# Kernel tuning notes

Hardware: AMD Instinct MI355X
Metric: run time of the kernel (lower is better)

## Reference

```python
import jax, jax.numpy as jnp
import numpy as np

N = 100000
E = 1600000
IN_FEATS = 256
OUT_FEATS = 256
EPS_WSUM = 1e-8   # clamp for weight sum
EPS_NORM = 1e-12  # F.normalize eps


def setup_inputs() -> dict:
    key = jax.random.key(0)
    k1, k2, k3, k4, k5 = jax.random.split(key, 5)
    x = jax.random.normal(k1, (N, IN_FEATS), dtype=jnp.float32)
    edge_index = jax.random.randint(k2, (2, E), 0, N, dtype=jnp.int64)
    edge_weight = jax.random.uniform(k3, (E,), dtype=jnp.float32)
    # Xavier-uniform-like init scale for [out, in] weights
    lim = float(np.sqrt(6.0 / (IN_FEATS + OUT_FEATS)) * np.sqrt(2.0))
    W_self = jax.random.uniform(k4, (OUT_FEATS, IN_FEATS), dtype=jnp.float32, minval=-lim, maxval=lim)
    W_neigh = jax.random.uniform(k5, (OUT_FEATS, IN_FEATS), dtype=jnp.float32, minval=-lim, maxval=lim)
    bias = jnp.zeros((OUT_FEATS,), dtype=jnp.float32)
    return {"x": x, "edge_index": edge_index, "edge_weight": edge_weight,
            "W_self": W_self, "W_neigh": W_neigh, "bias": bias}


def reference(x, edge_index, edge_weight, W_self, W_neigh, bias):
    row, col = edge_index[0], edge_index[1]
    # weighted mean aggregation: gather -> scale -> scatter-add -> normalize by weight sum
    weighted = x[row] * edge_weight[:, None]                       # [E, in]
    num = jax.ops.segment_sum(weighted, col, num_segments=N)       # [N, in]
    wsum = jax.ops.segment_sum(edge_weight, col, num_segments=N)   # [N]
    wsum = jnp.maximum(wsum, EPS_WSUM)
    neigh = num / wsum[:, None]                                    # [N, in]
    out = x @ W_self.T + neigh @ W_neigh.T + bias                  # [N, out]
    # L2 normalize (torch F.normalize semantics)
    nrm = jnp.maximum(jnp.linalg.norm(out, axis=-1, keepdims=True), EPS_NORM)
    return out / nrm
```

## Files before the change

### kernel.cpp

```cpp
#include <hip/hip_runtime.h>
#include <hip/hip_bf16.h>
#include <stdint.h>

#define IN_F 256
#define K_TOT 512
#define GR 64

typedef __attribute__((ext_vector_type(8))) _Float16 f16x8;
typedef __attribute__((ext_vector_type(4))) _Float16 f16x4;
typedef __attribute__((ext_vector_type(4))) float f32x4;
typedef __attribute__((ext_vector_type(2))) float f32x2;

#if __has_builtin(__builtin_amdgcn_cvt_pk_f32_fp8) && __has_builtin(__builtin_amdgcn_cvt_pk_fp8_f32)
#define HW_FP8 1
#endif

__device__ __forceinline__ float fp8_dec1(uint32_t b) {
  union { uint16_t u; _Float16 h; } cv;
  cv.u = (uint16_t)((b & 0x7F) << 7);
  float v = (float)cv.h * 256.0f;
  return (b & 0x80) ? -v : v;
}
__device__ __forceinline__ uint32_t fp8_enc1(float f) {
  union { _Float16 h; uint16_t u; } cv;
  cv.h = (_Float16)(f * (1.0f / 256.0f));
  uint32_t s = (cv.u >> 8) & 0x80;
  uint32_t t = cv.u & 0x7FFF;
  uint32_t r = (t + 0x3F + ((t >> 7) & 1)) >> 7;
  if (r > 0x7E) r = 0x7E;
  return s | r;
}
__device__ __forceinline__ void fp8x4_dec(uint32_t w, float4& o) {
#ifdef HW_FP8
  f32x2 lo = __builtin_amdgcn_cvt_pk_f32_fp8((int)w, false);
  f32x2 hi = __builtin_amdgcn_cvt_pk_f32_fp8((int)w, true);
  o.x = lo[0]; o.y = lo[1]; o.z = hi[0]; o.w = hi[1];
#else
  o.x = fp8_dec1(w & 0xFF); o.y = fp8_dec1((w >> 8) & 0xFF);
  o.z = fp8_dec1((w >> 16) & 0xFF); o.w = fp8_dec1(w >> 24);
#endif
}
__device__ __forceinline__ uint32_t fp8x4_enc(float a, float b, float c, float d) {
#ifdef HW_FP8
  int r = __builtin_amdgcn_cvt_pk_fp8_f32(a, b, 0, false);
  r = __builtin_amdgcn_cvt_pk_fp8_f32(c, d, r, true);
  return (uint32_t)r;
#else
  return fp8_enc1(a) | (fp8_enc1(b) << 8) | (fp8_enc1(c) << 16) | (fp8_enc1(d) << 24);
#endif
}

__global__ void init_kernel(const float* __restrict__ x,
                            const float* __restrict__ Ws,
                            const float* __restrict__ Wn,
                            const int* __restrict__ ei,
                            _Float16* __restrict__ Bhi,
                            uint32_t* __restrict__ xq, _Float16* __restrict__ Af16,
                            int* __restrict__ counts,
                            int* __restrict__ flag, int N, int nconv, int nmem) {
  __shared__ int bad_s[256];
  const int b = blockIdx.x;
  const int t = threadIdx.x;
  if (b < 512) {
    int idx = b * 256 + t;
    int j = idx >> 9;
    int k = idx & 511;
    float v = (k < IN_F) ? Ws[j * IN_F + k] : Wn[j * IN_F + (k - IN_F)];
    size_t addr = ((size_t)(k >> 5) * 256 + j) * 32 + (k & 31);
    Bhi[addr] = (_Float16)v;
  } else if (b < 512 + nconv) {
    size_t base = (size_t)(b - 512) * 4096 + (size_t)t * 16;
    size_t tot = (size_t)N * IN_F;
    if (base + 16 <= tot) {
      const float4* x4 = reinterpret_cast<const float4*>(x + base);
      float4 v0 = x4[0], v1 = x4[1], v2 = x4[2], v3 = x4[3];
      uint4 o;
      o.x = fp8x4_enc(v0.x, v0.y, v0.z, v0.w);
      o.y = fp8x4_enc(v1.x, v1.y, v1.z, v1.w);
      o.z = fp8x4_enc(v2.x, v2.y, v2.z, v2.w);
      o.w = fp8x4_enc(v3.x, v3.y, v3.z, v3.w);
      *reinterpret_cast<uint4*>(xq + base / 4) = o;
      size_t row = base >> 8;
      int col = (int)(base & 255);
      f16x8 h0 = {(_Float16)v0.x, (_Float16)v0.y, (_Float16)v0.z, (_Float16)v0.w,
                  (_Float16)v1.x, (_Float16)v1.y, (_Float16)v1.z, (_Float16)v1.w};
      f16x8 h1 = {(_Float16)v2.x, (_Float16)v2.y, (_Float16)v2.z, (_Float16)v2.w,
                  (_Float16)v3.x, (_Float16)v3.y, (_Float16)v3.z, (_Float16)v3.w};
      _Float16* dst = Af16 + row * K_TOT + col;
      *reinterpret_cast<f16x8*>(dst) = h0;
      *reinterpret_cast<f16x8*>(dst + 8) = h1;
    }
  } else if (b < 512 + nconv + nmem) {
    int base = (b - 512 - nconv) * 1024 + t * 4;
#pragma unroll
    for (int j = 0; j < 4; ++j)
      if (base + j < N) counts[base + j] = 0;
  } else {
    int bad = 0;
#pragma unroll
    for (int p = 0; p < 8; ++p) {
      int i = t + p * 256;
      if (ei[2 * i + 1] != 0) bad = 1;
    }
    bad_s[t] = bad;
    __syncthreads();
    for (int s = 128; s > 0; s >>= 1) {
      if (t < s) bad_s[t] |= bad_s[t + s];
      __syncthreads();
    }
    if (t == 0) *flag = (bad_s[0] == 0) ? 1 : 0;
  }
}

__global__ void hist_kernel(const int* __restrict__ ei, const int* __restrict__ flag,
                            int* __restrict__ counts, int E) {
  int e = blockIdx.x * 256 + threadIdx.x;
  if (e >= E) return;
  int is64 = *flag;
  int dst = is64 ? ei[2 * (E + e)] : ei[E + e];
  atomicAdd(counts + dst, 1);
}

__global__ void scan1_kernel(const int* __restrict__ counts, int* __restrict__ offsets,
                             int* __restrict__ bsums, int N) {
  __shared__ int buf[1024];
  int t = threadIdx.x;
  int i = blockIdx.x * 1024 + t;
  int v = (i < N) ? counts[i] : 0;
  buf[t] = v;
  __syncthreads();
  for (int s = 1; s < 1024; s <<= 1) {
    int add = (t >= s) ? buf[t - s] : 0;
    __syncthreads();
    buf[t] += add;
    __syncthreads();
  }
  if (i < N) offsets[i] = buf[t] - v;
  if (t == 1023) bsums[blockIdx.x] = buf[1023];
}

__global__ void scan23_kernel(int* __restrict__ offsets, const int* __restrict__ bsums,
                              int* __restrict__ cursor, int N, int E, int nb) {
  __shared__ int sb[128];
  int t = threadIdx.x;
  int v = 0;
  if (t < 128) {
    v = (t < nb) ? bsums[t] : 0;
    sb[t] = v;
  }
  __syncthreads();
  for (int s = 1; s < 128; s <<= 1) {
    int add = 0;
    if (t < 128 && t >= s) add = sb[t - s];
    __syncthreads();
    if (t < 128) sb[t] += add;
    __syncthreads();
  }
  if (t < 128) sb[t] -= v;
  __syncthreads();
  int i = blockIdx.x * 256 + t;
  if (i < N) {
    int o = offsets[i] + sb[i >> 10];
    offsets[i] = o;
    cursor[i] = o;
  }
  if (i == 0) offsets[N] = E;
}

__global__ void fill_kernel(const int* __restrict__ ei, const float* __restrict__ ew,
                            const int* __restrict__ flag, int* __restrict__ cursor,
                            uint32_t* __restrict__ edges, int E, int nper) {
  int q = blockIdx.x & 7;
  int e = (blockIdx.x >> 3) * 256 + threadIdx.x;
  if (e >= E) return;
  int is64 = *flag;
  int dst = is64 ? ei[2 * (E + e)] : ei[E + e];
  if (dst / nper != q) return;
  int src = is64 ? ei[2 * e] : ei[e];
  uint32_t w15 = (uint32_t)__float2int_rn(ew[e] * 32767.0f);
  int pos = atomicAdd(cursor + dst, 1);
  edges[pos] = ((uint32_t)src << 15) | w15;
}

__launch_bounds__(256)
__global__ void aggregate_fp8_kernel(const uint32_t* __restrict__ xq,
                                     const int* __restrict__ offsets,
                                     const uint32_t* __restrict__ edges,
                                     _Float16* __restrict__ Af16, int N) {
  int wid = blockIdx.x * 4 + (threadIdx.x >> 6);
  if (wid >= N) return;
  int lane = threadIdx.x & 63;
  int beg = offsets[wid];
  int end = offsets[wid + 1];
  float4 acc = {0.f, 0.f, 0.f, 0.f};
  float ws = 0.f;
  const float wscale = 1.0f / 32767.0f;
  int e = beg;
  for (; e + 3 < end; e += 4) {
    uint32_t n0 = edges[e], n1 = edges[e + 1], n2 = edges[e + 2], n3 = edges[e + 3];
    float w0 = (float)(n0 & 0x7FFF) * wscale, w1 = (float)(n1 & 0x7FFF) * wscale;
    float w2 = (float)(n2 & 0x7FFF) * wscale, w3 = (float)(n3 & 0x7FFF) * wscale;
    uint32_t q0 = xq[(size_t)(n0 >> 15) * 64 + lane];
    uint32_t q1 = xq[(size_t)(n1 >> 15) * 64 + lane];
    uint32_t q2 = xq[(size_t)(n2 >> 15) * 64 + lane];
    uint32_t q3 = xq[(size_t)(n3 >> 15) * 64 + lane];
    float4 f0, f1, f2, f3;
    fp8x4_dec(q0, f0); fp8x4_dec(q1, f1); fp8x4_dec(q2, f2); fp8x4_dec(q3, f3);
    acc.x += f0.x * w0 + f1.x * w1 + f2.x * w2 + f3.x * w3;
    acc.y += f0.y * w0 + f1.y * w1 + f2.y * w2 + f3.y * w3;
    acc.z += f0.z * w0 + f1.z * w1 + f2.z * w2 + f3.z * w3;
    acc.w += f0.w * w0 + f1.w * w1 + f2.w * w2 + f3.w * w3;
    ws += w0 + w1 + w2 + w3;
  }
  for (; e < end; ++e) {
    uint32_t n0 = edges[e];
    float w0 = (float)(n0 & 0x7FFF) * wscale;
    uint32_t q0 = xq[(size_t)(n0 >> 15) * 64 + lane];
    float4 f0;
    fp8x4_dec(q0, f0);
    acc.x += f0.x * w0; acc.y += f0.y * w0; acc.z += f0.z * w0; acc.w += f0.w * w0;
    ws += w0;
  }
  float inv = 1.f / fmaxf(ws, 1e-8f);
  f16x4 o = {(_Float16)(acc.x * inv), (_Float16)(acc.y * inv),
             (_Float16)(acc.z * inv), (_Float16)(acc.w * inv)};
  *reinterpret_cast<f16x4*>(Af16 + (size_t)wid * K_TOT + IN_F + lane * 4) = o;
}

__launch_bounds__(256)
__global__ void gemm_norm_kernel(const _Float16* __restrict__ Af16,
                                 const _Float16* __restrict__ Bhi,
                                 const float* __restrict__ bias,
                                 float* __restrict__ out, int N) {
  const int t = threadIdx.x;
  const int lane = t & 63;
  const int w = t >> 6;
  const int row0 = blockIdx.x * GR;

  __shared__ _Float16 Ah[2][256 * 8];
  __shared__ float ssb[GR][4];

  f32x4 acc[4][4];
#pragma unroll
  for (int rt = 0; rt < 4; ++rt)
#pragma unroll
    for (int ct = 0; ct < 4; ++ct) acc[rt][ct] = (f32x4){0.f, 0.f, 0.f, 0.f};

  int st_row = row0 + (t >> 6) * 16 + (t & 15);
  if (st_row >= N) st_row = N - 1;
  const _Float16* Abase = Af16 + (size_t)st_row * K_TOT + ((t >> 4) & 3) * 8;

  const size_t bfrag = (size_t)(w * 64 + (lane & 15)) * 32 + (lane >> 4) * 8;
  const _Float16* BhiP = Bhi + bfrag;

  *reinterpret_cast<f16x8*>(&Ah[0][t * 8]) = *reinterpret_cast<const f16x8*>(Abase);
  f16x8 a_next = *reinterpret_cast<const f16x8*>(Abase + 32);
  f16x8 bH[2][4];
#pragma unroll
  for (int ct = 0; ct < 4; ++ct) {
    bH[0][ct] = *reinterpret_cast<const f16x8*>(BhiP + ct * 512);
    bH[1][ct] = *reinterpret_cast<const f16x8*>(BhiP + 8192 + ct * 512);
  }
  __syncthreads();

#pragma unroll
  for (int ks = 0; ks < 16; ++ks) {
    f16x8 aH[4];
#pragma unroll
    for (int rt = 0; rt < 4; ++rt)
      aH[rt] = *reinterpret_cast<const f16x8*>(&Ah[ks & 1][(rt * 64 + lane) * 8]);
    f16x8 bNext[4];
    if (ks < 14) {
#pragma unroll
      for (int ct = 0; ct < 4; ++ct)
        bNext[ct] = *reinterpret_cast<const f16x8*>(BhiP + (size_t)(ks + 2) * 8192 + ct * 512);
    }
    if (ks < 15)
      *reinterpret_cast<f16x8*>(&Ah[(ks + 1) & 1][t * 8]) = a_next;
    if (ks < 14)
      a_next = *reinterpret_cast<const f16x8*>(Abase + (size_t)(ks + 2) * 32);
#pragma unroll
    for (int ct = 0; ct < 4; ++ct)
#pragma unroll
      for (int rt = 0; rt < 4; ++rt)
        acc[rt][ct] = __builtin_amdgcn_mfma_f32_16x16x32_f16(aH[rt], bH[ks & 1][ct], acc[rt][ct], 0, 0, 0);
    if (ks < 14) {
#pragma unroll
      for (int ct = 0; ct < 4; ++ct) bH[ks & 1][ct] = bNext[ct];
    }
    __syncthreads();
  }

  float bv[4];
#pragma unroll
  for (int ct = 0; ct < 4; ++ct) bv[ct] = bias[w * 64 + ct * 16 + (lane & 15)];

#pragma unroll
  for (int rt = 0; rt < 4; ++rt)
#pragma unroll
    for (int i = 0; i < 4; ++i) {
      float ssv = 0.f;
#pragma unroll
      for (int ct = 0; ct < 4; ++ct) {
        float val = acc[rt][ct][i] + bv[ct];
        acc[rt][ct][i] = val;
        ssv += val * val;
      }
#pragma unroll
      for (int s = 1; s < 16; s <<= 1) ssv += __shfl_xor(ssv, s, 64);
      if ((lane & 15) == 0) ssb[rt * 16 + (lane >> 4) * 4 + i][w] = ssv;
    }
  __syncthreads();

#pragma unroll
  for (int rt = 0; rt < 4; ++rt)
#pragma unroll
    for (int i = 0; i < 4; ++i) {
      int rl = rt * 16 + (lane >> 4) * 4 + i;
      f32x4 s4 = *reinterpret_cast<const f32x4*>(&ssb[rl][0]);
      float ss = s4[0] + s4[1] + s4[2] + s4[3];
      int gr = row0 + rl;
      if (gr < N) {
        float scale = 1.0f / fmaxf(sqrtf(ss), 1e-12f);
#pragma unroll
        for (int ct = 0; ct < 4; ++ct)
          out[(size_t)gr * IN_F + w * 64 + ct * 16 + (lane & 15)] = acc[rt][ct][i] * scale;
      }
    }
}

extern "C" void kernel_launch(void* const* d_in, const int* in_sizes, int n_in,
                              void* d_out, int out_size, void* d_ws, size_t ws_size,
                              hipStream_t stream) {
  const float* x = (const float*)d_in[0];
  const int* ei = (const int*)d_in[1];
  const float* ew = (const float*)d_in[2];
  const float* Wself = (const float*)d_in[3];
  const float* Wneigh = (const float*)d_in[4];
  const float* bias = (const float*)d_in[5];
  float* out = (float*)d_out;

  const int N = in_sizes[0] / IN_F;
  const int E = in_sizes[2];

  char* p = (char*)d_ws;
  _Float16* Af16 = (_Float16*)p;     p += (size_t)N * K_TOT * 2;
  _Float16* Bhi = (_Float16*)p;      p += (size_t)K_TOT * IN_F * 2;
  uint32_t* xq = (uint32_t*)p;       p += (size_t)N * IN_F;
  uint32_t* edges = (uint32_t*)p;    p += (size_t)E * 4;
  int* counts = (int*)p;             p += (size_t)N * 4;
  int* offsets = (int*)p;            p += (size_t)(N + 1) * 4;
  int* cursor = (int*)p;             p += (size_t)N * 4;
  int* bsums = (int*)p;              p += 128 * 4;
  int* flag = (int*)p;

  const int nconv = (int)(((size_t)N * IN_F + 4095) / 4096);
  const int nmem = (N + 1023) / 1024;
  const int nb = (N + 1023) / 1024;
  const int nper = (N + 7) / 8;

  init_kernel<<<512 + nconv + nmem + 1, 256, 0, stream>>>(
      x, Wself, Wneigh, ei, Bhi, xq, Af16, counts, flag, N, nconv, nmem);
  hist_kernel<<<(E + 255) / 256, 256, 0, stream>>>(ei, flag, counts, E);
  scan1_kernel<<<nb, 1024, 0, stream>>>(counts, offsets, bsums, N);
  scan23_kernel<<<(N + 255) / 256, 256, 0, stream>>>(offsets, bsums, cursor, N, E, nb);
  fill_kernel<<<((E + 255) / 256) * 8, 256, 0, stream>>>(ei, ew, flag, cursor, edges,
                                                         E, nper);
  aggregate_fp8_kernel<<<(N + 3) / 4, 256, 0, stream>>>(xq, offsets, edges, Af16, N);
  gemm_norm_kernel<<<(N + GR - 1) / GR, 256, 0, stream>>>(Af16, Bhi, bias, out, N);
}
```

Measured before the change: 302.8 us.

## Fuse neighbor aggregation into GEMM kernel, keeping aggregated rows in LDS

Merges the aggregation and GEMM+normalize kernels into one. Each block first aggregates neighbor features for its 64 rows into a shared-memory tile, then runs the MFMA GEMM reading the self half from fp32 x (converted to fp16 on the fly) and the neighbor half from LDS. This removes the fp16 Af16 intermediate buffer: its write in init, its write in aggregation, and its re-read in GEMM. The cost is that the gather phase runs with fewer resident waves per CU (GEMM-sized blocks with extra LDS), which can reduce latency hiding for the random xq loads. The gather loop is also unrolled to 8 edges per iteration.

```diff
diff --git a/kernel.cpp b/kernel.cpp
--- a/kernel.cpp
+++ b/kernel.cpp
@@ -55,7 +55,7 @@
                             const float* __restrict__ Wn,
                             const int* __restrict__ ei,
                             _Float16* __restrict__ Bhi,
-                            uint32_t* __restrict__ xq, _Float16* __restrict__ Af16,
+                            uint32_t* __restrict__ xq,
                             int* __restrict__ counts,
                             int* __restrict__ flag, int N, int nconv, int nmem) {
   __shared__ int bad_s[256];
@@ -80,15 +80,6 @@
       o.z = fp8x4_enc(v2.x, v2.y, v2.z, v2.w);
       o.w = fp8x4_enc(v3.x, v3.y, v3.z, v3.w);
       *reinterpret_cast<uint4*>(xq + base / 4) = o;
-      size_t row = base >> 8;
-      int col = (int)(base & 255);
-      f16x8 h0 = {(_Float16)v0.x, (_Float16)v0.y, (_Float16)v0.z, (_Float16)v0.w,
-                  (_Float16)v1.x, (_Float16)v1.y, (_Float16)v1.z, (_Float16)v1.w};
-      f16x8 h1 = {(_Float16)v2.x, (_Float16)v2.y, (_Float16)v2.z, (_Float16)v2.w,
-                  (_Float16)v3.x, (_Float16)v3.y, (_Float16)v3.z, (_Float16)v3.w};
-      _Float16* dst = Af16 + row * K_TOT + col;
-      *reinterpret_cast<f16x8*>(dst) = h0;
-      *reinterpret_cast<f16x8*>(dst + 8) = h1;
     }
   } else if (b < 512 + nconv + nmem) {
     int base = (b - 512 - nconv) * 1024 + t * 4;
@@ -183,62 +174,65 @@
 }
 
 __launch_bounds__(256)
-__global__ void aggregate_fp8_kernel(const uint32_t* __restrict__ xq,
-                                     const int* __restrict__ offsets,
-                                     const uint32_t* __restrict__ edges,
-                                     _Float16* __restrict__ Af16, int N) {
-  int wid = blockIdx.x * 4 + (threadIdx.x >> 6);
-  if (wid >= N) return;
-  int lane = threadIdx.x & 63;
-  int beg = offsets[wid];
-  int end = offsets[wid + 1];
-  float4 acc = {0.f, 0.f, 0.f, 0.f};
-  float ws = 0.f;
-  const float wscale = 1.0f / 32767.0f;
-  int e = beg;
-  for (; e + 3 < end; e += 4) {
-    uint32_t n0 = edges[e], n1 = edges[e + 1], n2 = edges[e + 2], n3 = edges[e + 3];
-    float w0 = (float)(n0 & 0x7FFF) * wscale, w1 = (float)(n1 & 0x7FFF) * wscale;
-    float w2 = (float)(n2 & 0x7FFF) * wscale, w3 = (float)(n3 & 0x7FFF) * wscale;
-    uint32_t q0 = xq[(size_t)(n0 >> 15) * 64 + lane];
-    uint32_t q1 = xq[(size_t)(n1 >> 15) * 64 + lane];
-    uint32_t q2 = xq[(size_t)(n2 >> 15) * 64 + lane];
-    uint32_t q3 = xq[(size_t)(n3 >> 15) * 64 + lane];
-    float4 f0, f1, f2, f3;
-    fp8x4_dec(q0, f0); fp8x4_dec(q1, f1); fp8x4_dec(q2, f2); fp8x4_dec(q3, f3);
-    acc.x += f0.x * w0 + f1.x * w1 + f2.x * w2 + f3.x * w3;
-    acc.y += f0.y * w0 + f1.y * w1 + f2.y * w2 + f3.y * w3;
-    acc.z += f0.z * w0 + f1.z * w1 + f2.z * w2 + f3.z * w3;
-    acc.w += f0.w * w0 + f1.w * w1 + f2.w * w2 + f3.w * w3;
-    ws += w0 + w1 + w2 + w3;
-  }
-  for (; e < end; ++e) {
-    uint32_t n0 = edges[e];
-    float w0 = (float)(n0 & 0x7FFF) * wscale;
-    uint32_t q0 = xq[(size_t)(n0 >> 15) * 64 + lane];
-    float4 f0;
-    fp8x4_dec(q0, f0);
-    acc.x += f0.x * w0; acc.y += f0.y * w0; acc.z += f0.z * w0; acc.w += f0.w * w0;
-    ws += w0;
-  }
-  float inv = 1.f / fmaxf(ws, 1e-8f);
-  f16x4 o = {(_Float16)(acc.x * inv), (_Float16)(acc.y * inv),
-             (_Float16)(acc.z * inv), (_Float16)(acc.w * inv)};
-  *reinterpret_cast<f16x4*>(Af16 + (size_t)wid * K_TOT + IN_F + lane * 4) = o;
-}
-
-__launch_bounds__(256)
-__global__ void gemm_norm_kernel(const _Float16* __restrict__ Af16,
-                                 const _Float16* __restrict__ Bhi,
-                                 const float* __restrict__ bias,
-                                 float* __restrict__ out, int N) {
+__global__ void agg_gemm_kernel(const float* __restrict__ x,
+                                const uint32_t* __restrict__ xq,
+                                const int* __restrict__ offsets,
+                                const uint32_t* __restrict__ edges,
+                                const _Float16* __restrict__ Bhi,
+                                const float* __restrict__ bias,
+                                float* __restrict__ out, int N) {
   const int t = threadIdx.x;
   const int lane = t & 63;
   const int w = t >> 6;
   const int row0 = blockIdx.x * GR;
 
-  __shared__ _Float16 Ah[2][256 * 8];
+  __shared__ _Float16 neighT[GR][264];
+  __shared__ _Float16 Adb[2][256 * 8];
   __shared__ float ssb[GR][4];
+
+  const float wscale = 1.0f / 32767.0f;
+  for (int r = 0; r < 16; ++r) {
+    int node = row0 + w * 16 + r;
+    float4 acc = {0.f, 0.f, 0.f, 0.f};
+    float ws = 0.f;
+    if (node < N) {
+      int beg = offsets[node];
+      int end = offsets[node + 1];
+      int e = beg;
+      for (; e + 7 < end; e += 8) {
+        uint32_t n[8];
+#pragma unroll
+        for (int j = 0; j < 8; ++j) n[j] = edges[e + j];
+        uint32_t q[8];
+#pragma unroll
+        for (int j = 0; j < 8; ++j)
+          q[j] = xq[(size_t)(n[j] >> 15) * 64 + lane];
+#pragma unroll
+        for (int j = 0; j < 8; ++j) {
+          float wj = (float)(n[j] & 0x7FFF) * wscale;
+          float4 fj;
+          fp8x4_dec(q[j], fj);
+          acc.x += fj.x * wj; acc.y += fj.y * wj;
+          acc.z += fj.z * wj; acc.w += fj.w * wj;
+          ws += wj;
+        }
+      }
+      for (; e < end; ++e) {
+        uint32_t n0 = edges[e];
+        float w0 = (float)(n0 & 0x7FFF) * wscale;
+        uint32_t q0 = xq[(size_t)(n0 >> 15) * 64 + lane];
+        float4 f0;
+        fp8x4_dec(q0, f0);
+        acc.x += f0.x * w0; acc.y += f0.y * w0;
+        acc.z += f0.z * w0; acc.w += f0.w * w0;
+        ws += w0;
+      }
+      float inv = 1.f / fmaxf(ws, 1e-8f);
+      acc.x *= inv; acc.y *= inv; acc.z *= inv; acc.w *= inv;
+    }
+    f16x4 o = {(_Float16)acc.x, (_Float16)acc.y, (_Float16)acc.z, (_Float16)acc.w};
+    *reinterpret_cast<f16x4*>(&neighT[w * 16 + r][lane * 4]) = o;
+  }
 
   f32x4 acc[4][4];
 #pragma unroll
@@ -248,13 +242,25 @@
 
   int st_row = row0 + (t >> 6) * 16 + (t & 15);
   if (st_row >= N) st_row = N - 1;
-  const _Float16* Abase = Af16 + (size_t)st_row * K_TOT + ((t >> 4) & 3) * 8;
+  const float* Ax = x + (size_t)st_row * IN_F + ((t >> 4) & 3) * 8;
 
   const size_t bfrag = (size_t)(w * 64 + (lane & 15)) * 32 + (lane >> 4) * 8;
   const _Float16* BhiP = Bhi + bfrag;
 
-  *reinterpret_cast<f16x8*>(&Ah[0][t * 8]) = *reinterpret_cast<const f16x8*>(Abase);
-  f16x8 a_next = *reinterpret_cast<const f16x8*>(Abase + 32);
+  {
+    float4 va = *reinterpret_cast<const float4*>(Ax);
+    float4 vb = *reinterpret_cast<const float4*>(Ax + 4);
+    f16x8 hv = {(_Float16)va.x, (_Float16)va.y, (_Float16)va.z, (_Float16)va.w,
+                (_Float16)vb.x, (_Float16)vb.y, (_Float16)vb.z, (_Float16)vb.w};
+    *reinterpret_cast<f16x8*>(&Adb[0][t * 8]) = hv;
+  }
+  f16x8 a_next;
+  {
+    float4 va = *reinterpret_cast<const float4*>(Ax + 32);
+    float4 vb = *reinterpret_cast<const float4*>(Ax + 36);
+    a_next = (f16x8){(_Float16)va.x, (_Float16)va.y, (_Float16)va.z, (_Float16)va.w,
+                     (_Float16)vb.x, (_Float16)vb.y, (_Float16)vb.z, (_Float16)vb.w};
+  }
   f16x8 bH[2][4];
 #pragma unroll
   for (int ct = 0; ct < 4; ++ct) {
@@ -266,35 +272,48 @@
 #pragma unroll
   for (int ks = 0; ks < 16; ++ks) {
     f16x8 aH[4];
-#pragma unroll
-    for (int rt = 0; rt < 4; ++rt)
-      aH[rt] = *reinterpret_cast<const f16x8*>(&Ah[ks & 1][(rt * 64 + lane) * 8]);
+    if (ks < 8) {
+#pragma unroll
+      for (int rt = 0; rt < 4; ++rt)
+        aH[rt] = *reinterpret_cast<const f16x8*>(&Adb[ks & 1][(rt * 64 + lane) * 8]);
+    } else {
+#pragma unroll
+      for (int rt = 0; rt < 4; ++rt)
+        aH[rt] = *reinterpret_cast<const f16x8*>(
+            &neighT[rt * 16 + (lane & 15)][(ks - 8) * 32 + (lane >> 4) * 8]);
+    }
     f16x8 bNext[4];
     if (ks < 14) {
 #pragma unroll
       for (int ct = 0; ct < 4; ++ct)
         bNext[ct] = *reinterpret_cast<const f16x8*>(BhiP + (size_t)(ks + 2) * 8192 + ct * 512);
     }
-    if (ks < 15)
-      *reinterpret_cast<f16x8*>(&Ah[(ks + 1) & 1][t * 8]) = a_next;
-    if (ks < 14)
-      a_next = *reinterpret_cast<const f16x8*>(Abase + (size_t)(ks + 2) * 32);
+    if (ks < 7)
+      *reinterpret_cast<f16x8*>(&Adb[(ks + 1) & 1][t * 8]) = a_next;
+    if (ks < 6) {
+      float4 va = *reinterpret_cast<const float4*>(Ax + (size_t)(ks + 2) * 32);
+      float4 vb = *reinterpret_cast<const float4*>(Ax + (size_t)(ks + 2) * 32 + 4);
+      a_next = (f16x8){(_Float16)va.x, (_Float16)va.y, (_Float16)va.z, (_Float16)va.w,
+                       (_Float16)vb.x, (_Float16)vb.y, (_Float16)vb.z, (_Float16)vb.w};
+    }
 #pragma unroll
     for (int ct = 0; ct < 4; ++ct)
 #pragma unroll
       for (int rt = 0; rt < 4; ++rt)
-        acc[rt][ct] = __builtin_amdgcn_mfma_f32_16x16x32_f16(aH[rt], bH[ks & 1][ct], acc[rt][ct], 0, 0, 0);
+        acc[rt][ct] = __builtin_amdgcn_mfma_f32_16x16x32_f16(aH[rt], bH[ks & 1][ct],
+                                                             acc[rt][ct], 0, 0, 0);
     if (ks < 14) {
 #pragma unroll
       for (int ct = 0; ct < 4; ++ct) bH[ks & 1][ct] = bNext[ct];
     }
-    __syncthreads();
+    if (ks < 7) __syncthreads();
   }
 
   float bv[4];
 #pragma unroll
   for (int ct = 0; ct < 4; ++ct) bv[ct] = bias[w * 64 + ct * 16 + (lane & 15)];
 
+  __syncthreads();
 #pragma unroll
   for (int rt = 0; rt < 4; ++rt)
 #pragma unroll
@@ -344,7 +363,6 @@
   const int E = in_sizes[2];
 
   char* p = (char*)d_ws;
-  _Float16* Af16 = (_Float16*)p;     p += (size_t)N * K_TOT * 2;
   _Float16* Bhi = (_Float16*)p;      p += (size_t)K_TOT * IN_F * 2;
   uint32_t* xq = (uint32_t*)p;       p += (size_t)N * IN_F;
   uint32_t* edges = (uint32_t*)p;    p += (size_t)E * 4;
@@ -360,12 +378,12 @@
   const int nper = (N + 7) / 8;
 
   init_kernel<<<512 + nconv + nmem + 1, 256, 0, stream>>>(
-      x, Wself, Wneigh, ei, Bhi, xq, Af16, counts, flag, N, nconv, nmem);
+      x, Wself, Wneigh, ei, Bhi, xq, counts, flag, N, nconv, nmem);
   hist_kernel<<<(E + 255) / 256, 256, 0, stream>>>(ei, flag, counts, E);
   scan1_kernel<<<nb, 1024, 0, stream>>>(counts, offsets, bsums, N);
   scan23_kernel<<<(N + 255) / 256, 256, 0, stream>>>(offsets, bsums, cursor, N, E, nb);
   fill_kernel<<<((E + 255) / 256) * 8, 256, 0, stream>>>(ei, ew, flag, cursor, edges,
                                                          E, nper);
-  aggregate_fp8_kernel<<<(N + 3) / 4, 256, 0, stream>>>(xq, offsets, edges, Af16, N);
-  gemm_norm_kernel<<<(N + GR - 1) / GR, 256, 0, stream>>>(Af16, Bhi, bias, out, N);
-}
+  agg_gemm_kernel<<<(N + GR - 1) / GR, 256, 0, stream>>>(x, xq, offsets, edges, Bhi,
+                                                         bias, out, N);
+}
```

New measurement: 376.8 us. +24.4%, slower.

## Fold histogram into init kernel and preload full A panel in GEMM

Applied to the files above, without the earlier changes.

The histogram pass moves into the init kernel: each hist block recomputes the int64 flag locally and does the atomic counting, and the counts zeroing becomes a hipMemsetAsync. This removes one kernel launch and the dependency on the flag buffer. The GEMM now loads the whole 64x512 fp16 A tile into a 64KB LDS panel up front and drops the per-k-step __syncthreads and double buffering. In exchange, every hist block repeats the flag reduction, and the larger LDS use lowers occupancy while giving up the overlap of A loads with MFMA work.

```diff
diff --git a/kernel.cpp b/kernel.cpp
--- a/kernel.cpp
+++ b/kernel.cpp
@@ -57,7 +57,8 @@
                             _Float16* __restrict__ Bhi,
                             uint32_t* __restrict__ xq, _Float16* __restrict__ Af16,
                             int* __restrict__ counts,
-                            int* __restrict__ flag, int N, int nconv, int nmem) {
+                            int* __restrict__ flag, int N, int E,
+                            int nconv, int nhist) {
   __shared__ int bad_s[256];
   const int b = blockIdx.x;
   const int t = threadIdx.x;
@@ -90,11 +91,23 @@
       *reinterpret_cast<f16x8*>(dst) = h0;
       *reinterpret_cast<f16x8*>(dst + 8) = h1;
     }
-  } else if (b < 512 + nconv + nmem) {
-    int base = (b - 512 - nconv) * 1024 + t * 4;
-#pragma unroll
-    for (int j = 0; j < 4; ++j)
-      if (base + j < N) counts[base + j] = 0;
+  } else if (b < 512 + nconv + nhist) {
+    int bad = 0;
+#pragma unroll
+    for (int p = 0; p < 8; ++p)
+      if (ei[2 * (t + p * 256) + 1] != 0) bad = 1;
+    bad_s[t] = bad;
+    __syncthreads();
+    for (int s = 128; s > 0; s >>= 1) {
+      if (t < s) bad_s[t] |= bad_s[t + s];
+      __syncthreads();
+    }
+    int is64 = (bad_s[0] == 0);
+    int e = (b - 512 - nconv) * 256 + t;
+    if (e < E) {
+      int dst = is64 ? ei[2 * (E + e)] : ei[E + e];
+      atomicAdd(counts + dst, 1);
+    }
   } else {
     int bad = 0;
 #pragma unroll
@@ -110,15 +123,6 @@
     }
     if (t == 0) *flag = (bad_s[0] == 0) ? 1 : 0;
   }
-}
-
-__global__ void hist_kernel(const int* __restrict__ ei, const int* __restrict__ flag,
-                            int* __restrict__ counts, int E) {
-  int e = blockIdx.x * 256 + threadIdx.x;
-  if (e >= E) return;
-  int is64 = *flag;
-  int dst = is64 ? ei[2 * (E + e)] : ei[E + e];
-  atomicAdd(counts + dst, 1);
 }
 
 __global__ void scan1_kernel(const int* __restrict__ counts, int* __restrict__ offsets,
@@ -237,7 +241,7 @@
   const int w = t >> 6;
   const int row0 = blockIdx.x * GR;
 
-  __shared__ _Float16 Ah[2][256 * 8];
+  __shared__ _Float16 Apan[4096 * 8];
   __shared__ float ssb[GR][4];
 
   f32x4 acc[4][4];
@@ -253,8 +257,11 @@
   const size_t bfrag = (size_t)(w * 64 + (lane & 15)) * 32 + (lane >> 4) * 8;
   const _Float16* BhiP = Bhi + bfrag;
 
-  *reinterpret_cast<f16x8*>(&Ah[0][t * 8]) = *reinterpret_cast<const f16x8*>(Abase);
-  f16x8 a_next = *reinterpret_cast<const f16x8*>(Abase + 32);
+#pragma unroll
+  for (int ks = 0; ks < 16; ++ks)
+    *reinterpret_cast<f16x8*>(&Apan[(ks * 256 + t) * 8]) =
+        *reinterpret_cast<const f16x8*>(Abase + ks * 32);
+
   f16x8 bH[2][4];
 #pragma unroll
   for (int ct = 0; ct < 4; ++ct) {
@@ -268,27 +275,24 @@
     f16x8 aH[4];
 #pragma unroll
     for (int rt = 0; rt < 4; ++rt)
-      aH[rt] = *reinterpret_cast<const f16x8*>(&Ah[ks & 1][(rt * 64 + lane) * 8]);
+      aH[rt] = *reinterpret_cast<const f16x8*>(
+          &Apan[(ks * 256 + rt * 64 + lane) * 8]);
     f16x8 bNext[4];
     if (ks < 14) {
 #pragma unroll
       for (int ct = 0; ct < 4; ++ct)
         bNext[ct] = *reinterpret_cast<const f16x8*>(BhiP + (size_t)(ks + 2) * 8192 + ct * 512);
     }
-    if (ks < 15)
-      *reinterpret_cast<f16x8*>(&Ah[(ks + 1) & 1][t * 8]) = a_next;
-    if (ks < 14)
-      a_next = *reinterpret_cast<const f16x8*>(Abase + (size_t)(ks + 2) * 32);
 #pragma unroll
     for (int ct = 0; ct < 4; ++ct)
 #pragma unroll
       for (int rt = 0; rt < 4; ++rt)
-        acc[rt][ct] = __builtin_amdgcn_mfma_f32_16x16x32_f16(aH[rt], bH[ks & 1][ct], acc[rt][ct], 0, 0, 0);
+        acc[rt][ct] = __builtin_amdgcn_mfma_f32_16x16x32_f16(aH[rt], bH[ks & 1][ct],
+                                                             acc[rt][ct], 0, 0, 0);
     if (ks < 14) {
 #pragma unroll
       for (int ct = 0; ct < 4; ++ct) bH[ks & 1][ct] = bNext[ct];
     }
-    __syncthreads();
   }
 
   float bv[4];
@@ -355,13 +359,14 @@
   int* flag = (int*)p;
 
   const int nconv = (int)(((size_t)N * IN_F + 4095) / 4096);
-  const int nmem = (N + 1023) / 1024;
+  const int nhist = (E + 255) / 256;
   const int nb = (N + 1023) / 1024;
   const int nper = (N + 7) / 8;
 
-  init_kernel<<<512 + nconv + nmem + 1, 256, 0, stream>>>(
-      x, Wself, Wneigh, ei, Bhi, xq, Af16, counts, flag, N, nconv, nmem);
-  hist_kernel<<<(E + 255) / 256, 256, 0, stream>>>(ei, flag, counts, E);
+  hipMemsetAsync(counts, 0, (size_t)N * sizeof(int), stream);
+
+  init_kernel<<<512 + nconv + nhist + 1, 256, 0, stream>>>(
+      x, Wself, Wneigh, ei, Bhi, xq, Af16, counts, flag, N, E, nconv, nhist);
   scan1_kernel<<<nb, 1024, 0, stream>>>(counts, offsets, bsums, N);
   scan23_kernel<<<(N + 255) / 256, 256, 0, stream>>>(offsets, bsums, cursor, N, E, nb);
   fill_kernel<<<((E + 255) / 256) * 8, 256, 0, stream>>>(ei, ew, flag, cursor, edges,
```

Measured after the change: 331.6 us. +9.5%, slower.
